# Kernel tuning notes

Hardware: AMD Instinct MI355X
Metric: run time of the kernel (lower is better)

## Reference

```python
import jax, jax.numpy as jnp
import numpy as np

B, T, D_E, D_RHO = 4, 2048, 8, 8
D_MODEL, NHEAD, NLAYERS, DFF = 128, 4, 3, 256
WINDOW = 64
LN_EPS = 1e-5


def _layernorm(x, g, b):
    mu = jnp.mean(x, axis=-1, keepdims=True)
    var = jnp.mean((x - mu) ** 2, axis=-1, keepdims=True)
    return (x - mu) * jax.lax.rsqrt(var + LN_EPS) * g + b


def _pos_encoding(t, d, dtype):
    half = d // 2
    pos = jnp.arange(t, dtype=dtype)[:, None]
    div = jnp.exp(jnp.arange(half, dtype=dtype) * (-jnp.log(jnp.asarray(10000.0, dtype)) / half))
    ang = pos * div[None, :]  # (T, half)
    pe = jnp.zeros((t, d), dtype=dtype)
    pe = pe.at[:, 0:2 * half:2].set(jnp.sin(ang))
    pe = pe.at[:, 1:2 * half:2].set(jnp.cos(ang))
    return pe[None]  # (1, T, d)


def setup_inputs() -> dict:
    key = jax.random.key(0)
    ks = iter(jax.random.split(key, 32))
    d_in = D_E + D_RHO

    def lin(k, fan_in, shape):
        return jax.random.uniform(k, shape, jnp.float32, -1.0, 1.0) / np.sqrt(fan_in)

    inp = {
        'E': jax.random.normal(next(ks), (B, T, D_E), jnp.float32),
        'rho_side': jax.random.normal(next(ks), (B, T, D_RHO), jnp.float32),
        'W_in1': lin(next(ks), d_in, (d_in, D_MODEL)), 'b_in1': jnp.zeros((D_MODEL,)),
        'W_in2': lin(next(ks), D_MODEL, (D_MODEL, D_MODEL)), 'b_in2': jnp.zeros((D_MODEL,)),
        'Wqkv': lin(next(ks), D_MODEL, (NLAYERS, D_MODEL, 3 * D_MODEL)), 'bqkv': jnp.zeros((NLAYERS, 3 * D_MODEL)),
        'Wo': lin(next(ks), D_MODEL, (NLAYERS, D_MODEL, D_MODEL)), 'bo': jnp.zeros((NLAYERS, D_MODEL)),
        'ln1_g': jnp.ones((NLAYERS, D_MODEL)), 'ln1_b': jnp.zeros((NLAYERS, D_MODEL)),
        'Wff1': lin(next(ks), D_MODEL, (NLAYERS, D_MODEL, DFF)), 'bff1': jnp.zeros((NLAYERS, DFF)),
        'Wff2': lin(next(ks), DFF, (NLAYERS, DFF, D_MODEL)), 'bff2': jnp.zeros((NLAYERS, D_MODEL)),
        'ln2_g': jnp.ones((NLAYERS, D_MODEL)), 'ln2_b': jnp.zeros((NLAYERS, D_MODEL)),
        'W_head': lin(next(ks), D_MODEL, (D_MODEL, D_RHO)), 'b_head': jnp.zeros((D_RHO,)),
    }
    return inp


def reference(E, rho_side, W_in1, b_in1, W_in2, b_in2, Wqkv, bqkv, Wo, bo,
              ln1_g, ln1_b, Wff1, bff1, Wff2, bff2, ln2_g, ln2_b, W_head, b_head):
    b, t, _ = E.shape
    x = jnp.concatenate([E, rho_side], axis=-1)  # (B,T,d_e+d_rho)
    # in_proj: Linear -> ReLU -> Linear, then add sinusoidal PE (layernorm_in=False)
    h = jax.nn.relu(x @ W_in1 + b_in1) @ W_in2 + b_in2
    h = h + _pos_encoding(t, D_MODEL, h.dtype)

    # banded causal mask: blocked if j > i or j < i - window + 1 (additive -inf)
    i = jnp.arange(t)[:, None]
    j = jnp.arange(t)[None, :]
    blocked = (j > i) | (j < i - WINDOW + 1)
    bias = jnp.where(blocked, -jnp.inf, 0.0).astype(h.dtype)[None, None]  # (1,1,T,T)

    hd = D_MODEL // NHEAD
    scale = 1.0 / np.sqrt(hd)
    for l in range(NLAYERS):
        # --- self-attention (post-norm TransformerEncoderLayer, dropout=0) ---
        qkv = h @ Wqkv[l] + bqkv[l]
        q, k, v = jnp.split(qkv, 3, axis=-1)
        q = q.reshape(b, t, NHEAD, hd)
        k = k.reshape(b, t, NHEAD, hd)
        v = v.reshape(b, t, NHEAD, hd)
        scores = jnp.einsum('bqhd,bkhd->bhqk', q, k) * scale + bias
        attn = jax.nn.softmax(scores, axis=-1)
        o = jnp.einsum('bhqk,bkhd->bqhd', attn, v).reshape(b, t, D_MODEL)
        h = _layernorm(h + o @ Wo[l] + bo[l], ln1_g[l], ln1_b[l])
        # --- feed-forward ---
        ff = jax.nn.relu(h @ Wff1[l] + bff1[l]) @ Wff2[l] + bff2[l]
        h = _layernorm(h + ff, ln2_g[l], ln2_b[l])

    return h @ W_head + b_head  # (B,T,d_rho)
```

## Files before the change

### kernel.cpp

```cpp
#include <hip/hip_runtime.h>
#include <hip/hip_bf16.h>
#include <math.h>

#define TSEQ 2048
#define NBATCH 4
#define NTOK (TSEQ * NBATCH)
#define DM 128
#define WIN 64
#define DFF 256
#define NQKV 384
#define QT 64

typedef __attribute__((ext_vector_type(8))) short bf16x8;
typedef __attribute__((ext_vector_type(4))) float f32x4;

__device__ __forceinline__ unsigned short f2bf(float f) {
    union { float f; unsigned int u; } v; v.f = f;
    unsigned int r = v.u + 0x7fffu + ((v.u >> 16) & 1u);
    return (unsigned short)(r >> 16);
}
__device__ __forceinline__ float bf2f_lo(unsigned int u) {
    union { unsigned int u; float f; } v; v.u = u << 16; return v.f;
}
__device__ __forceinline__ float bf2f_hi(unsigned int u) {
    union { unsigned int u; float f; } v; v.u = u & 0xffff0000u; return v.f;
}

__global__ void k_wconv(const float* __restrict__ Wqkv, const float* __restrict__ Wo,
                        const float* __restrict__ Wff1, const float* __restrict__ Wff2,
                        unsigned short* __restrict__ wq, unsigned short* __restrict__ wo,
                        unsigned short* __restrict__ w1, unsigned short* __restrict__ w2) {
    int idx = blockIdx.x * 256 + threadIdx.x;
    const int s1 = 3 * 128 * 384, s2 = 3 * 128 * 128, s3 = 3 * 128 * 256, s4 = 3 * 256 * 128;
    if (idx < s1) {
        int l = idx / (384 * 128), rem = idx % (384 * 128);
        int n = rem / 128, k = rem % 128;
        wq[idx] = f2bf(Wqkv[(size_t)l * 128 * 384 + k * 384 + n]);
    } else if ((idx -= s1) < s2) {
        int l = idx / (128 * 128), rem = idx % (128 * 128);
        int n = rem / 128, k = rem % 128;
        wo[idx] = f2bf(Wo[(size_t)l * 128 * 128 + k * 128 + n]);
    } else if ((idx -= s2) < s3) {
        int l = idx / (256 * 128), rem = idx % (256 * 128);
        int n = rem / 128, k = rem % 128;
        w1[idx] = f2bf(Wff1[(size_t)l * 128 * 256 + k * 256 + n]);
    } else if ((idx -= s3) < s4) {
        int l = idx / (128 * 256), rem = idx % (128 * 256);
        int n = rem / 256, k = rem % 256;
        w2[idx] = f2bf(Wff2[(size_t)l * 256 * 128 + k * 128 + n]);
    }
}

template<int ROWS>
__global__ void k_inproj(const float* __restrict__ E, const float* __restrict__ rho,
                         const float* __restrict__ W1, const float* __restrict__ b1,
                         const float* __restrict__ W2, const float* __restrict__ b2,
                         float* __restrict__ h, unsigned short* __restrict__ hbf) {
    const int row0 = blockIdx.x * ROWS;
    const int tid = threadIdx.x;
    __shared__ float x[ROWS][16];
    __shared__ float h1[ROWS][DM];

    for (int idx = tid; idx < ROWS * 16; idx += DM) {
        int r = idx >> 4, c = idx & 15;
        int tok = row0 + r;
        x[r][c] = (c < 8) ? E[(size_t)tok * 8 + c] : rho[(size_t)tok * 8 + (c - 8)];
    }
    __syncthreads();

    float acc[ROWS];
#pragma unroll
    for (int r = 0; r < ROWS; ++r) acc[r] = b1[tid];
    for (int k = 0; k < 16; ++k) {
        float w = W1[k * DM + tid];
#pragma unroll
        for (int r = 0; r < ROWS; ++r) acc[r] += x[r][k] * w;
    }
#pragma unroll
    for (int r = 0; r < ROWS; ++r) h1[r][tid] = fmaxf(acc[r], 0.f);
    __syncthreads();

#pragma unroll
    for (int r = 0; r < ROWS; ++r) acc[r] = b2[tid];
    for (int k = 0; k < DM; ++k) {
        float w = W2[k * DM + tid];
#pragma unroll
        for (int r = 0; r < ROWS; ++r) acc[r] += h1[r][k] * w;
    }

    const float c0 = -0.14391156831212787f;
    float dv = __expf(c0 * (float)(tid >> 1));
#pragma unroll
    for (int r = 0; r < ROWS; ++r) {
        int tok = row0 + r;
        int t = tok & (TSEQ - 1);
        float ang = (float)t * dv;
        float pe = (tid & 1) ? cosf(ang) : sinf(ang);
        float v = acc[r] + pe;
        h[(size_t)tok * DM + tid] = v;
        hbf[(size_t)tok * DM + tid] = f2bf(v);
    }
}

template<int K, int N, bool RELU, bool OUTBF16>
__global__ __launch_bounds__(256) void k_gemm_mfma(
        const unsigned short* __restrict__ A,
        const unsigned short* __restrict__ Wt,
        const float* __restrict__ bias,
        void* __restrict__ Cout) {
    const int bm0 = blockIdx.x * 64;
    const int bn0 = blockIdx.y * 64;
    const int w = threadIdx.x >> 6;
    const int l = threadIdx.x & 63;
    const int lr = l & 15;
    const int lk = l >> 4;
    const int arow = bm0 + w * 16 + lr;

    bf16x8 aF[K / 32];
    const unsigned short* ap = A + (size_t)arow * K + lk * 8;
#pragma unroll
    for (int ks = 0; ks < K / 32; ++ks)
        aF[ks] = *(const bf16x8*)(ap + ks * 32);

    f32x4 acc[4];
#pragma unroll
    for (int nt = 0; nt < 4; ++nt) {
        float b = bias[bn0 + nt * 16 + lr];
        acc[nt][0] = b; acc[nt][1] = b; acc[nt][2] = b; acc[nt][3] = b;
    }

#pragma unroll
    for (int ks = 0; ks < K / 32; ++ks) {
#pragma unroll
        for (int nt = 0; nt < 4; ++nt) {
            const unsigned short* bp = Wt + (size_t)(bn0 + nt * 16 + lr) * K + ks * 32 + lk * 8;
            bf16x8 bF = *(const bf16x8*)bp;
            acc[nt] = __builtin_amdgcn_mfma_f32_16x16x32_bf16(aF[ks], bF, acc[nt], 0, 0, 0);
        }
    }

#pragma unroll
    for (int nt = 0; nt < 4; ++nt) {
        int col = bn0 + nt * 16 + lr;
#pragma unroll
        for (int r = 0; r < 4; ++r) {
            int row = bm0 + w * 16 + lk * 4 + r;
            float v = acc[nt][r];
            if (RELU) v = fmaxf(v, 0.f);
            if (OUTBF16) ((unsigned short*)Cout)[(size_t)row * N + col] = f2bf(v);
            else ((float*)Cout)[(size_t)row * N + col] = v;
        }
    }
}

template<int K>
__global__ __launch_bounds__(128) void k_gemm_ln(
        const unsigned short* __restrict__ A,
        const unsigned short* __restrict__ Wt,
        const float* __restrict__ bias,
        const float* __restrict__ g, const float* __restrict__ be,
        float* __restrict__ h, unsigned short* __restrict__ hbf) {
    const int bm0 = blockIdx.x * 32;
    const int w = threadIdx.x >> 6;
    const int l = threadIdx.x & 63;
    const int lr = l & 15;
    const int lk = l >> 4;
    const int arow = bm0 + w * 16 + lr;

    bf16x8 aF[K / 32];
    const unsigned short* ap = A + (size_t)arow * K + lk * 8;
#pragma unroll
    for (int ks = 0; ks < K / 32; ++ks)
        aF[ks] = *(const bf16x8*)(ap + ks * 32);

    f32x4 acc[8];
#pragma unroll
    for (int nt = 0; nt < 8; ++nt) {
        float b = bias[nt * 16 + lr];
        acc[nt][0] = b; acc[nt][1] = b; acc[nt][2] = b; acc[nt][3] = b;
    }

#pragma unroll
    for (int ks = 0; ks < K / 32; ++ks) {
#pragma unroll
        for (int nt = 0; nt < 8; ++nt) {
            const unsigned short* bp = Wt + (size_t)(nt * 16 + lr) * K + ks * 32 + lk * 8;
            bf16x8 bF = *(const bf16x8*)bp;
            acc[nt] = __builtin_amdgcn_mfma_f32_16x16x32_bf16(aF[ks], bF, acc[nt], 0, 0, 0);
        }
    }

#pragma unroll
    for (int nt = 0; nt < 8; ++nt) {
        int col = nt * 16 + lr;
#pragma unroll
        for (int r = 0; r < 4; ++r) {
            int row = bm0 + w * 16 + lk * 4 + r;
            acc[nt][r] += h[(size_t)row * DM + col];
        }
    }

    float s[4], s2[4];
#pragma unroll
    for (int r = 0; r < 4; ++r) {
        float a0 = 0.f, a1 = 0.f;
#pragma unroll
        for (int nt = 0; nt < 8; ++nt) { a0 += acc[nt][r]; a1 += acc[nt][r] * acc[nt][r]; }
        s[r] = a0; s2[r] = a1;
    }
#pragma unroll
    for (int off = 8; off; off >>= 1) {
#pragma unroll
        for (int r = 0; r < 4; ++r) {
            s[r]  += __shfl_xor(s[r],  off);
            s2[r] += __shfl_xor(s2[r], off);
        }
    }
    float mean[4], rstd[4];
#pragma unroll
    for (int r = 0; r < 4; ++r) {
        mean[r] = s[r] * (1.f / DM);
        float var = s2[r] * (1.f / DM) - mean[r] * mean[r];
        rstd[r] = rsqrtf(var + 1e-5f);
    }

#pragma unroll
    for (int nt = 0; nt < 8; ++nt) {
        int col = nt * 16 + lr;
        float gg = g[col], bb = be[col];
#pragma unroll
        for (int r = 0; r < 4; ++r) {
            int row = bm0 + w * 16 + lk * 4 + r;
            float v = (acc[nt][r] - mean[r]) * rstd[r] * gg + bb;
            h[(size_t)row * DM + col] = v;
            hbf[(size_t)row * DM + col] = f2bf(v);
        }
    }
}

__global__ __launch_bounds__(128) void k_ff_fused(
        const unsigned short* __restrict__ A,
        const unsigned short* __restrict__ W1t,
        const float* __restrict__ b1,
        const unsigned short* __restrict__ W2t,
        const float* __restrict__ b2,
        const float* __restrict__ g, const float* __restrict__ be,
        float* __restrict__ h, unsigned short* __restrict__ hbf) {
    const int bm0 = blockIdx.x * 32;
    const int w = threadIdx.x >> 6;
    const int l = threadIdx.x & 63;
    const int lr = l & 15;
    const int lk = l >> 4;

    __shared__ unsigned short a2[32][264];

    const int arow = bm0 + w * 16 + lr;
    bf16x8 aF[4];
    const unsigned short* ap = A + (size_t)arow * DM + lk * 8;
#pragma unroll
    for (int ks = 0; ks < 4; ++ks)
        aF[ks] = *(const bf16x8*)(ap + ks * 32);

    f32x4 acc[16];
#pragma unroll
    for (int nt = 0; nt < 16; ++nt) { acc[nt][0] = 0.f; acc[nt][1] = 0.f; acc[nt][2] = 0.f; acc[nt][3] = 0.f; }

#pragma unroll
    for (int ks = 0; ks < 4; ++ks) {
#pragma unroll
        for (int nt = 0; nt < 16; ++nt) {
            const unsigned short* wp = W1t + (size_t)(nt * 16 + lr) * DM + ks * 32 + lk * 8;
            bf16x8 wF = *(const bf16x8*)wp;
            acc[nt] = __builtin_amdgcn_mfma_f32_16x16x32_bf16(wF, aF[ks], acc[nt], 0, 0, 0);
        }
    }

    const int mloc = w * 16 + lr;
#pragma unroll
    for (int nt = 0; nt < 16; ++nt) {
        int n0 = nt * 16 + lk * 4;
        uint2 pk;
        float v0 = fmaxf(acc[nt][0] + b1[n0 + 0], 0.f);
        float v1 = fmaxf(acc[nt][1] + b1[n0 + 1], 0.f);
        float v2 = fmaxf(acc[nt][2] + b1[n0 + 2], 0.f);
        float v3 = fmaxf(acc[nt][3] + b1[n0 + 3], 0.f);
        pk.x = (unsigned int)f2bf(v0) | ((unsigned int)f2bf(v1) << 16);
        pk.y = (unsigned int)f2bf(v2) | ((unsigned int)f2bf(v3) << 16);
        *(uint2*)&a2[mloc][n0] = pk;
    }
    __syncthreads();

    bf16x8 aF2[8];
#pragma unroll
    for (int ks = 0; ks < 8; ++ks)
        aF2[ks] = *(const bf16x8*)&a2[w * 16 + lr][ks * 32 + lk * 8];

    f32x4 acc2[8];
#pragma unroll
    for (int nt = 0; nt < 8; ++nt) {
        float b = b2[nt * 16 + lr];
        acc2[nt][0] = b; acc2[nt][1] = b; acc2[nt][2] = b; acc2[nt][3] = b;
    }

#pragma unroll
    for (int ks = 0; ks < 8; ++ks) {
#pragma unroll
        for (int nt = 0; nt < 8; ++nt) {
            const unsigned short* bp = W2t + (size_t)(nt * 16 + lr) * DFF + ks * 32 + lk * 8;
            bf16x8 bF = *(const bf16x8*)bp;
            acc2[nt] = __builtin_amdgcn_mfma_f32_16x16x32_bf16(aF2[ks], bF, acc2[nt], 0, 0, 0);
        }
    }

#pragma unroll
    for (int nt = 0; nt < 8; ++nt) {
        int col = nt * 16 + lr;
#pragma unroll
        for (int r = 0; r < 4; ++r) {
            int row = bm0 + w * 16 + lk * 4 + r;
            acc2[nt][r] += h[(size_t)row * DM + col];
        }
    }

    float s[4], s2[4];
#pragma unroll
    for (int r = 0; r < 4; ++r) {
        float a0 = 0.f, a1 = 0.f;
#pragma unroll
        for (int nt = 0; nt < 8; ++nt) { a0 += acc2[nt][r]; a1 += acc2[nt][r] * acc2[nt][r]; }
        s[r] = a0; s2[r] = a1;
    }
#pragma unroll
    for (int off = 8; off; off >>= 1) {
#pragma unroll
        for (int r = 0; r < 4; ++r) {
            s[r]  += __shfl_xor(s[r],  off);
            s2[r] += __shfl_xor(s2[r], off);
        }
    }
    float mean[4], rstd[4];
#pragma unroll
    for (int r = 0; r < 4; ++r) {
        mean[r] = s[r] * (1.f / DM);
        float var = s2[r] * (1.f / DM) - mean[r] * mean[r];
        rstd[r] = rsqrtf(var + 1e-5f);
    }

#pragma unroll
    for (int nt = 0; nt < 8; ++nt) {
        int col = nt * 16 + lr;
        float gg = g[col], bb = be[col];
#pragma unroll
        for (int r = 0; r < 4; ++r) {
            int row = bm0 + w * 16 + lk * 4 + r;
            float v = (acc2[nt][r] - mean[r]) * rstd[r] * gg + bb;
            h[(size_t)row * DM + col] = v;
            hbf[(size_t)row * DM + col] = f2bf(v);
        }
    }
}

__global__ void k_attn2(const unsigned short* __restrict__ qkv, unsigned short* __restrict__ o) {
    const int t0   = blockIdx.x * QT;
    const int head = blockIdx.y;
    const int b    = blockIdx.z;
    const int tid  = threadIdx.x;
    const int q    = tid >> 2;
    const int s    = tid & 3;

    __shared__ float kbuf[127][36];
    __shared__ float vbuf[127][36];

    for (int idx = tid; idx < 127 * 4; idx += 256) {
        int kb = idx >> 2, c = idx & 3;
        int j = t0 - 63 + kb;
        uint4 kv = make_uint4(0, 0, 0, 0), vv = make_uint4(0, 0, 0, 0);
        if (j >= 0) {
            const unsigned short* base = qkv + ((size_t)(b * TSEQ + j)) * NQKV + head * 32 + c * 8;
            kv = *(const uint4*)(base + 128);
            vv = *(const uint4*)(base + 256);
        }
        float* kd = &kbuf[kb][c * 8];
        float* vd = &vbuf[kb][c * 8];
        kd[0] = bf2f_lo(kv.x); kd[1] = bf2f_hi(kv.x); kd[2] = bf2f_lo(kv.y); kd[3] = bf2f_hi(kv.y);
        kd[4] = bf2f_lo(kv.z); kd[5] = bf2f_hi(kv.z); kd[6] = bf2f_lo(kv.w); kd[7] = bf2f_hi(kv.w);
        vd[0] = bf2f_lo(vv.x); vd[1] = bf2f_hi(vv.x); vd[2] = bf2f_lo(vv.y); vd[3] = bf2f_hi(vv.y);
        vd[4] = bf2f_lo(vv.z); vd[5] = bf2f_hi(vv.z); vd[6] = bf2f_lo(vv.w); vd[7] = bf2f_hi(vv.w);
    }

    float qreg[32];
    {
        const unsigned short* qp = qkv + ((size_t)(b * TSEQ + t0 + q)) * NQKV + head * 32;
#pragma unroll
        for (int c = 0; c < 4; ++c) {
            uint4 u = *(const uint4*)(qp + c * 8);
            float* qd = &qreg[c * 8];
            qd[0] = bf2f_lo(u.x); qd[1] = bf2f_hi(u.x); qd[2] = bf2f_lo(u.y); qd[3] = bf2f_hi(u.y);
            qd[4] = bf2f_lo(u.z); qd[5] = bf2f_hi(u.z); qd[6] = bf2f_lo(u.w); qd[7] = bf2f_hi(u.w);
        }
    }
    __syncthreads();

    const float scale = 0.17677669529663687f;
    float sc[16];
#pragma unroll
    for (int kk = 0; kk < 16; ++kk) {
        int w = s + 4 * kk;
        int kb = q + w;
        float acc = 0.f;
#pragma unroll
        for (int d = 0; d < 32; ++d) acc += qreg[d] * kbuf[kb][d];
        int j = t0 + q - 63 + w;
        sc[kk] = (j >= 0) ? acc * scale : -1e30f;
    }

    float m = sc[0];
#pragma unroll
    for (int kk = 1; kk < 16; ++kk) m = fmaxf(m, sc[kk]);
    m = fmaxf(m, __shfl_xor(m, 1));
    m = fmaxf(m, __shfl_xor(m, 2));
    float sum = 0.f;
#pragma unroll
    for (int kk = 0; kk < 16; ++kk) { sc[kk] = __expf(sc[kk] - m); sum += sc[kk]; }
    sum += __shfl_xor(sum, 1);
    sum += __shfl_xor(sum, 2);
    const float inv = 1.f / sum;

    float acc[32];
#pragma unroll
    for (int d = 0; d < 32; ++d) acc[d] = 0.f;
#pragma unroll
    for (int kk = 0; kk < 16; ++kk) {
        float p = sc[kk] * inv;
        int kb = q + s + 4 * kk;
#pragma unroll
        for (int d = 0; d < 32; ++d) acc[d] += p * vbuf[kb][d];
    }
#pragma unroll
    for (int d = 0; d < 32; ++d) {
        acc[d] += __shfl_xor(acc[d], 1);
        acc[d] += __shfl_xor(acc[d], 2);
    }
    if (s == 0) {
        unsigned short* op = o + ((size_t)(b * TSEQ + t0 + q)) * DM + head * 32;
#pragma unroll
        for (int d = 0; d < 32; d += 2) {
            unsigned int u = ((unsigned int)f2bf(acc[d + 1]) << 16) | f2bf(acc[d]);
            *(unsigned int*)(op + d) = u;
        }
    }
}

__global__ void k_head(const float* __restrict__ h, const float* __restrict__ W,
                       const float* __restrict__ bias, float* __restrict__ out) {
    const int tok = blockIdx.x * blockDim.x + threadIdx.x;
    if (tok >= NTOK) return;
    float acc[8];
#pragma unroll
    for (int r = 0; r < 8; ++r) acc[r] = bias[r];
    for (int k = 0; k < DM; ++k) {
        float hv = h[(size_t)tok * DM + k];
#pragma unroll
        for (int r = 0; r < 8; ++r) acc[r] += hv * W[k * 8 + r];
    }
#pragma unroll
    for (int r = 0; r < 8; ++r) out[(size_t)tok * 8 + r] = acc[r];
}

extern "C" void kernel_launch(void* const* d_in, const int* in_sizes, int n_in,
                              void* d_out, int out_size, void* d_ws, size_t ws_size,
                              hipStream_t stream) {
    const float* E     = (const float*)d_in[0];
    const float* rho   = (const float*)d_in[1];
    const float* W_in1 = (const float*)d_in[2];
    const float* b_in1 = (const float*)d_in[3];
    const float* W_in2 = (const float*)d_in[4];
    const float* b_in2 = (const float*)d_in[5];
    const float* Wqkv  = (const float*)d_in[6];
    const float* bqkv  = (const float*)d_in[7];
    const float* Wo    = (const float*)d_in[8];
    const float* bo    = (const float*)d_in[9];
    const float* ln1g  = (const float*)d_in[10];
    const float* ln1b  = (const float*)d_in[11];
    const float* Wff1  = (const float*)d_in[12];
    const float* bff1  = (const float*)d_in[13];
    const float* Wff2  = (const float*)d_in[14];
    const float* bff2  = (const float*)d_in[15];
    const float* ln2g  = (const float*)d_in[16];
    const float* ln2b  = (const float*)d_in[17];
    const float* Whead = (const float*)d_in[18];
    const float* bhead = (const float*)d_in[19];
    float* out = (float*)d_out;

    char* ws = (char*)d_ws;
    const size_t MB = 1024 * 1024;
    float*          h    = (float*)ws;
    unsigned short* hbf  = (unsigned short*)(ws + 4 * MB);
    unsigned short* obf  = (unsigned short*)(ws + 6 * MB);
    unsigned short* wq   = (unsigned short*)(ws + 8 * MB);
    unsigned short* wo   = (unsigned short*)(ws + 8 * MB + 294912);
    unsigned short* w1   = (unsigned short*)(ws + 8 * MB + 294912 + 98304);
    unsigned short* w2   = (unsigned short*)(ws + 8 * MB + 294912 + 98304 + 196608);
    unsigned short* qkvb = (unsigned short*)(ws + 9 * MB);

    constexpr int ROWS = 8;
    k_wconv<<<1536, 256, 0, stream>>>(Wqkv, Wo, Wff1, Wff2, wq, wo, w1, w2);
    k_inproj<ROWS><<<NTOK / ROWS, DM, 0, stream>>>(E, rho, W_in1, b_in1, W_in2, b_in2, h, hbf);
    for (int l = 0; l < 3; ++l) {
        k_gemm_mfma<DM, NQKV, false, true><<<dim3(NTOK / 64, NQKV / 64), 256, 0, stream>>>(
            hbf, wq + (size_t)l * NQKV * DM, bqkv + l * NQKV, qkvb);
        k_attn2<<<dim3(TSEQ / QT, 4, NBATCH), 256, 0, stream>>>(qkvb, obf);
        k_gemm_ln<DM><<<NTOK / 32, 128, 0, stream>>>(
            obf, wo + (size_t)l * DM * DM, bo + l * DM, ln1g + l * DM, ln1b + l * DM, h, hbf);
        k_ff_fused<<<NTOK / 32, 128, 0, stream>>>(
            hbf, w1 + (size_t)l * DFF * DM, bff1 + l * DFF,
            w2 + (size_t)l * DM * DFF, bff2 + l * DM,
            ln2g + l * DM, ln2b + l * DM, h, hbf);
    }
    k_head<<<NTOK / 256, 256, 0, stream>>>(h, Whead, bhead, out);
}
```

Measured before the change: 288.7 us.

## Fuse windowed attention with output projection, residual and layernorm

Merges the attention kernel and the Wo GEMM+residual+LayerNorm kernel into a single kernel. Each block handles 32 query rows across all 4 heads and keeps the attention output in shared memory instead of writing it to global. This removes one launch per layer and the global round-trip of the attention output. In exchange, the K/V halo is now loaded for 95 rows per 32 queries instead of 127 per 64, the grid has fewer, larger blocks, and only 128 of the 512 threads do the GEMM/LN tail while the rest sit idle.

```diff
diff --git a/kernel.cpp b/kernel.cpp
--- a/kernel.cpp
+++ b/kernel.cpp
@@ -9,7 +9,6 @@
 #define WIN 64
 #define DFF 256
 #define NQKV 384
-#define QT 64
 
 typedef __attribute__((ext_vector_type(8))) short bf16x8;
 typedef __attribute__((ext_vector_type(4))) float f32x4;
@@ -153,91 +152,6 @@
     }
 }
 
-template<int K>
-__global__ __launch_bounds__(128) void k_gemm_ln(
-        const unsigned short* __restrict__ A,
-        const unsigned short* __restrict__ Wt,
-        const float* __restrict__ bias,
-        const float* __restrict__ g, const float* __restrict__ be,
-        float* __restrict__ h, unsigned short* __restrict__ hbf) {
-    const int bm0 = blockIdx.x * 32;
-    const int w = threadIdx.x >> 6;
-    const int l = threadIdx.x & 63;
-    const int lr = l & 15;
-    const int lk = l >> 4;
-    const int arow = bm0 + w * 16 + lr;
-
-    bf16x8 aF[K / 32];
-    const unsigned short* ap = A + (size_t)arow * K + lk * 8;
-#pragma unroll
-    for (int ks = 0; ks < K / 32; ++ks)
-        aF[ks] = *(const bf16x8*)(ap + ks * 32);
-
-    f32x4 acc[8];
-#pragma unroll
-    for (int nt = 0; nt < 8; ++nt) {
-        float b = bias[nt * 16 + lr];
-        acc[nt][0] = b; acc[nt][1] = b; acc[nt][2] = b; acc[nt][3] = b;
-    }
-
-#pragma unroll
-    for (int ks = 0; ks < K / 32; ++ks) {
-#pragma unroll
-        for (int nt = 0; nt < 8; ++nt) {
-            const unsigned short* bp = Wt + (size_t)(nt * 16 + lr) * K + ks * 32 + lk * 8;
-            bf16x8 bF = *(const bf16x8*)bp;
-            acc[nt] = __builtin_amdgcn_mfma_f32_16x16x32_bf16(aF[ks], bF, acc[nt], 0, 0, 0);
-        }
-    }
-
-#pragma unroll
-    for (int nt = 0; nt < 8; ++nt) {
-        int col = nt * 16 + lr;
-#pragma unroll
-        for (int r = 0; r < 4; ++r) {
-            int row = bm0 + w * 16 + lk * 4 + r;
-            acc[nt][r] += h[(size_t)row * DM + col];
-        }
-    }
-
-    float s[4], s2[4];
-#pragma unroll
-    for (int r = 0; r < 4; ++r) {
-        float a0 = 0.f, a1 = 0.f;
-#pragma unroll
-        for (int nt = 0; nt < 8; ++nt) { a0 += acc[nt][r]; a1 += acc[nt][r] * acc[nt][r]; }
-        s[r] = a0; s2[r] = a1;
-    }
-#pragma unroll
-    for (int off = 8; off; off >>= 1) {
-#pragma unroll
-        for (int r = 0; r < 4; ++r) {
-            s[r]  += __shfl_xor(s[r],  off);
-            s2[r] += __shfl_xor(s2[r], off);
-        }
-    }
-    float mean[4], rstd[4];
-#pragma unroll
-    for (int r = 0; r < 4; ++r) {
-        mean[r] = s[r] * (1.f / DM);
-        float var = s2[r] * (1.f / DM) - mean[r] * mean[r];
-        rstd[r] = rsqrtf(var + 1e-5f);
-    }
-
-#pragma unroll
-    for (int nt = 0; nt < 8; ++nt) {
-        int col = nt * 16 + lr;
-        float gg = g[col], bb = be[col];
-#pragma unroll
-        for (int r = 0; r < 4; ++r) {
-            int row = bm0 + w * 16 + lk * 4 + r;
-            float v = (acc[nt][r] - mean[r]) * rstd[r] * gg + bb;
-            h[(size_t)row * DM + col] = v;
-            hbf[(size_t)row * DM + col] = f2bf(v);
-        }
-    }
-}
-
 __global__ __launch_bounds__(128) void k_ff_fused(
         const unsigned short* __restrict__ A,
         const unsigned short* __restrict__ W1t,
@@ -360,37 +274,40 @@
     }
 }
 
-__global__ void k_attn2(const unsigned short* __restrict__ qkv, unsigned short* __restrict__ o) {
-    const int t0   = blockIdx.x * QT;
-    const int head = blockIdx.y;
-    const int b    = blockIdx.z;
-    const int tid  = threadIdx.x;
-    const int q    = tid >> 2;
-    const int s    = tid & 3;
-
-    __shared__ float kbuf[127][36];
-    __shared__ float vbuf[127][36];
-
-    for (int idx = tid; idx < 127 * 4; idx += 256) {
-        int kb = idx >> 2, c = idx & 3;
+__global__ __launch_bounds__(512) void k_attn_ln(
+        const unsigned short* __restrict__ qkv,
+        const unsigned short* __restrict__ Wt,
+        const float* __restrict__ bias,
+        const float* __restrict__ g, const float* __restrict__ be,
+        float* __restrict__ h, unsigned short* __restrict__ hbf) {
+    const int t0 = blockIdx.x * 32;
+    const int b  = blockIdx.y;
+    const int tid = threadIdx.x;
+
+    __shared__ float kbuf[4][95][33];
+    __shared__ float vbuf[4][95][33];
+    __shared__ unsigned short obuf[32][136];
+
+    for (int idx = tid; idx < 95 * 32; idx += 512) {
+        int kb = idx >> 5, c = idx & 31;
         int j = t0 - 63 + kb;
-        uint4 kv = make_uint4(0, 0, 0, 0), vv = make_uint4(0, 0, 0, 0);
-        if (j >= 0) {
-            const unsigned short* base = qkv + ((size_t)(b * TSEQ + j)) * NQKV + head * 32 + c * 8;
-            kv = *(const uint4*)(base + 128);
-            vv = *(const uint4*)(base + 256);
-        }
-        float* kd = &kbuf[kb][c * 8];
-        float* vd = &vbuf[kb][c * 8];
-        kd[0] = bf2f_lo(kv.x); kd[1] = bf2f_hi(kv.x); kd[2] = bf2f_lo(kv.y); kd[3] = bf2f_hi(kv.y);
-        kd[4] = bf2f_lo(kv.z); kd[5] = bf2f_hi(kv.z); kd[6] = bf2f_lo(kv.w); kd[7] = bf2f_hi(kv.w);
-        vd[0] = bf2f_lo(vv.x); vd[1] = bf2f_hi(vv.x); vd[2] = bf2f_lo(vv.y); vd[3] = bf2f_hi(vv.y);
-        vd[4] = bf2f_lo(vv.z); vd[5] = bf2f_hi(vv.z); vd[6] = bf2f_lo(vv.w); vd[7] = bf2f_hi(vv.w);
-    }
+        int isV = c >> 4;
+        int c2 = c & 15;
+        uint4 u = make_uint4(0, 0, 0, 0);
+        if (j >= 0)
+            u = *(const uint4*)(qkv + ((size_t)(b * TSEQ + j)) * NQKV + 128 + isV * 128 + c2 * 8);
+        float* dst = isV ? &vbuf[c2 >> 2][kb][(c2 & 3) * 8] : &kbuf[c2 >> 2][kb][(c2 & 3) * 8];
+        dst[0] = bf2f_lo(u.x); dst[1] = bf2f_hi(u.x); dst[2] = bf2f_lo(u.y); dst[3] = bf2f_hi(u.y);
+        dst[4] = bf2f_lo(u.z); dst[5] = bf2f_hi(u.z); dst[6] = bf2f_lo(u.w); dst[7] = bf2f_hi(u.w);
+    }
+
+    const int q  = tid >> 4;
+    const int hh = (tid >> 2) & 3;
+    const int s  = tid & 3;
 
     float qreg[32];
     {
-        const unsigned short* qp = qkv + ((size_t)(b * TSEQ + t0 + q)) * NQKV + head * 32;
+        const unsigned short* qp = qkv + ((size_t)(b * TSEQ + t0 + q)) * NQKV + hh * 32;
 #pragma unroll
         for (int c = 0; c < 4; ++c) {
             uint4 u = *(const uint4*)(qp + c * 8);
@@ -407,11 +324,11 @@
     for (int kk = 0; kk < 16; ++kk) {
         int w = s + 4 * kk;
         int kb = q + w;
-        float acc = 0.f;
-#pragma unroll
-        for (int d = 0; d < 32; ++d) acc += qreg[d] * kbuf[kb][d];
+        float a = 0.f;
+#pragma unroll
+        for (int d = 0; d < 32; ++d) a += qreg[d] * kbuf[hh][kb][d];
         int j = t0 + q - 63 + w;
-        sc[kk] = (j >= 0) ? acc * scale : -1e30f;
+        sc[kk] = (j >= 0) ? a * scale : -1e30f;
     }
 
     float m = sc[0];
@@ -434,7 +351,7 @@
         float p = sc[kk] * inv;
         int kb = q + s + 4 * kk;
 #pragma unroll
-        for (int d = 0; d < 32; ++d) acc[d] += p * vbuf[kb][d];
+        for (int d = 0; d < 32; ++d) acc[d] += p * vbuf[hh][kb][d];
     }
 #pragma unroll
     for (int d = 0; d < 32; ++d) {
@@ -442,11 +359,88 @@
         acc[d] += __shfl_xor(acc[d], 2);
     }
     if (s == 0) {
-        unsigned short* op = o + ((size_t)(b * TSEQ + t0 + q)) * DM + head * 32;
 #pragma unroll
         for (int d = 0; d < 32; d += 2) {
             unsigned int u = ((unsigned int)f2bf(acc[d + 1]) << 16) | f2bf(acc[d]);
-            *(unsigned int*)(op + d) = u;
+            *(unsigned int*)&obuf[q][hh * 32 + d] = u;
+        }
+    }
+    __syncthreads();
+
+    if (tid < 128) {
+        const int w = tid >> 6;
+        const int l = tid & 63;
+        const int lr = l & 15;
+        const int lk = l >> 4;
+        const size_t rbase = (size_t)(b * TSEQ + t0);
+
+        bf16x8 aF[4];
+#pragma unroll
+        for (int ks = 0; ks < 4; ++ks)
+            aF[ks] = *(const bf16x8*)&obuf[w * 16 + lr][ks * 32 + lk * 8];
+
+        f32x4 acc2[8];
+#pragma unroll
+        for (int nt = 0; nt < 8; ++nt) {
+            float bb = bias[nt * 16 + lr];
+            acc2[nt][0] = bb; acc2[nt][1] = bb; acc2[nt][2] = bb; acc2[nt][3] = bb;
+        }
+
+#pragma unroll
+        for (int ks = 0; ks < 4; ++ks) {
+#pragma unroll
+            for (int nt = 0; nt < 8; ++nt) {
+                const unsigned short* bp = Wt + (size_t)(nt * 16 + lr) * DM + ks * 32 + lk * 8;
+                bf16x8 bF = *(const bf16x8*)bp;
+                acc2[nt] = __builtin_amdgcn_mfma_f32_16x16x32_bf16(aF[ks], bF, acc2[nt], 0, 0, 0);
+            }
+        }
+
+#pragma unroll
+        for (int nt = 0; nt < 8; ++nt) {
+            int col = nt * 16 + lr;
+#pragma unroll
+            for (int r = 0; r < 4; ++r) {
+                size_t row = rbase + w * 16 + lk * 4 + r;
+                acc2[nt][r] += h[row * DM + col];
+            }
+        }
+
+        float sA[4], sB[4];
+#pragma unroll
+        for (int r = 0; r < 4; ++r) {
+            float a0 = 0.f, a1 = 0.f;
+#pragma unroll
+            for (int nt = 0; nt < 8; ++nt) { a0 += acc2[nt][r]; a1 += acc2[nt][r] * acc2[nt][r]; }
+            sA[r] = a0; sB[r] = a1;
+        }
+#pragma unroll
+        for (int off = 8; off; off >>= 1) {
+#pragma unroll
+            for (int r = 0; r < 4; ++r) {
+                sA[r] += __shfl_xor(sA[r], off);
+                sB[r] += __shfl_xor(sB[r], off);
+            }
+        }
+        float mean[4], rstd[4];
+#pragma unroll
+        for (int r = 0; r < 4; ++r) {
+            mean[r] = sA[r] * (1.f / DM);
+            float var = sB[r] * (1.f / DM) - mean[r] * mean[r];
+            rstd[r] = rsqrtf(var + 1e-5f);
+        }
+
+#pragma unroll
+        for (int nt = 0; nt < 8; ++nt) {
+            int col = nt * 16 + lr;
+            float gg = g[col], bb2 = be[col];
+#pragma unroll
+            for (int r = 0; r < 4; ++r) {
+                size_t row = rbase + w * 16 + lk * 4 + r;
+                float v = (acc2[nt][r] - mean[r]) * rstd[r] * gg + bb2;
+                h[row * DM + col] = v;
+                hbf[row * DM + col] = f2bf(v);
+            }
         }
     }
 }
@@ -496,7 +490,6 @@
     const size_t MB = 1024 * 1024;
     float*          h    = (float*)ws;
     unsigned short* hbf  = (unsigned short*)(ws + 4 * MB);
-    unsigned short* obf  = (unsigned short*)(ws + 6 * MB);
     unsigned short* wq   = (unsigned short*)(ws + 8 * MB);
     unsigned short* wo   = (unsigned short*)(ws + 8 * MB + 294912);
     unsigned short* w1   = (unsigned short*)(ws + 8 * MB + 294912 + 98304);
@@ -509,9 +502,8 @@
     for (int l = 0; l < 3; ++l) {
         k_gemm_mfma<DM, NQKV, false, true><<<dim3(NTOK / 64, NQKV / 64), 256, 0, stream>>>(
             hbf, wq + (size_t)l * NQKV * DM, bqkv + l * NQKV, qkvb);
-        k_attn2<<<dim3(TSEQ / QT, 4, NBATCH), 256, 0, stream>>>(qkvb, obf);
-        k_gemm_ln<DM><<<NTOK / 32, 128, 0, stream>>>(
-            obf, wo + (size_t)l * DM * DM, bo + l * DM, ln1g + l * DM, ln1b + l * DM, h, hbf);
+        k_attn_ln<<<dim3(TSEQ / 32, NBATCH), 512, 0, stream>>>(
+            qkvb, wo + (size_t)l * DM * DM, bo + l * DM, ln1g + l * DM, ln1b + l * DM, h, hbf);
         k_ff_fused<<<NTOK / 32, 128, 0, stream>>>(
             hbf, w1 + (size_t)l * DFF * DM, bff1 + l * DFF,
             w2 + (size_t)l * DM * DFF, bff2 + l * DM,
```

Result: slower. 308.6 us (+6.9%).
